# Optimization experiments

Hardware: AMD Instinct MI355X
Metric: run time of the kernel (lower is better)

Reference implementation:

```python
import jax, jax.numpy as jnp
import numpy as np

R_FACTOR = 5  # reduction factor r from Tacotron.__init__


def _gru(x, h, Wx, Wh, b):
    # standard GRU cell: z,r,candidate gates packed along last dim of Wx/Wh/b
    H = h.shape[-1]
    gx = x @ Wx
    gh = h @ Wh
    z = jax.nn.sigmoid(gx[..., :H] + gh[..., :H] + b[:H])
    r = jax.nn.sigmoid(gx[..., H:2 * H] + gh[..., H:2 * H] + b[H:2 * H])
    c = jnp.tanh(gx[..., 2 * H:] + r * gh[..., 2 * H:] + b[2 * H:])
    return (1.0 - z) * h + z * c


def setup_inputs() -> dict:
    key = jax.random.key(0)
    ks = jax.random.split(key, 16)
    T_out, B, D = 1000, 128, 80     # decoder frames, batch, mel dim
    T_in, H, P = 512, 256, 128      # encoder steps, hidden, prenet out
    n = lambda k, shp, d: jax.random.normal(k, shp, dtype=jnp.float32) * (1.0 / np.sqrt(d))
    return {
        "outputs": jax.random.normal(ks[0], (T_out, B, D), dtype=jnp.float32),
        "memory": jax.random.normal(ks[1], (T_in, B, H), dtype=jnp.float32),
        "W_pre0": n(ks[2], (D, H), D), "b_pre0": jnp.zeros((H,), jnp.float32),
        "W_pre1": n(ks[3], (H, P), H), "b_pre1": jnp.zeros((P,), jnp.float32),
        "Wx_att": n(ks[4], (P, 3 * H), P), "Wh_att": n(ks[5], (H, 3 * H), H), "b_att": jnp.zeros((3 * H,), jnp.float32),
        "Wq": n(ks[6], (H, H), H), "Wm": n(ks[7], (H, H), H), "v_att": n(ks[8], (H,), H),
        "Wx_d0": n(ks[9], (2 * H, 3 * H), 2 * H), "Wh_d0": n(ks[10], (H, 3 * H), H), "b_d0": jnp.zeros((3 * H,), jnp.float32),
        "Wx_d1": n(ks[11], (H, 3 * H), H), "Wh_d1": n(ks[12], (H, 3 * H), H), "b_d1": jnp.zeros((3 * H,), jnp.float32),
        "Wo": n(ks[13], (H, D), H), "bo": jnp.zeros((D,), jnp.float32),
    }


def _forward(outputs, memory, W_pre0, b_pre0, W_pre1, b_pre1, Wx_att, Wh_att, b_att,
             Wq, Wm, v_att, Wx_d0, Wh_d0, b_d0, Wx_d1, Wh_d1, b_d1, Wo, bo):
    r = R_FACTOR
    T_out, B, D = outputs.shape
    H = memory.shape[-1]
    R = T_out // r  # reduced_time_steps
    # teacher-forcing frame per reduced step: indic[t*r + r - 1] with r zero-frames
    # prepended == outputs[t*r - 1] for t>=1, zeros for t=0.
    frames = jnp.concatenate(
        [jnp.zeros((1, B, D), outputs.dtype), outputs[r - 1::r][: R - 1]], axis=0)  # [R,B,D]
    # precompute attention keys once (AttModule over static memory)
    keys = jnp.einsum('tbh,hk->tbk', memory, Wm)  # [T_in,B,H]
    h0 = jnp.zeros((B, H), outputs.dtype)

    def step(state, frame):
        h_att, h_d0, h_d1 = state
        # pre-net (dropout inactive: inference-mode reference)
        pre = jax.nn.relu(frame @ W_pre0 + b_pre0)
        pre = jax.nn.relu(pre @ W_pre1 + b_pre1)
        # attention RNN
        query = _gru(pre, h_att, Wx_att, Wh_att, b_att)  # [B,H]
        # additive attention
        e = jnp.einsum('tbk,k->tb', jnp.tanh(keys + query @ Wq), v_att)  # [T_in,B]
        alpha = jax.nn.softmax(e, axis=0)
        context = jnp.einsum('tb,tbh->bh', alpha, memory)  # [B,H]
        # decoder cell 0 conditioned on context, with residual from query
        out0 = _gru(jnp.concatenate([query, context], axis=-1), h_d0, Wx_d0, Wh_d0, b_d0)
        res0 = query + out0
        # residual-wrapped decoder cell 1
        out1 = _gru(res0, h_d1, Wx_d1, Wh_d1, b_d1)
        res1 = res0 + out1
        dense = res1 @ Wo + bo  # [B,D]
        return (query, out0, out1), (dense, alpha)

    _, (dense_seq, alpha_seq) = jax.lax.scan(step, (h0, h0, h0), frames)
    # each reduced-step output is written to r consecutive output frames
    final_output = jnp.repeat(dense_seq, r, axis=0)  # [T_out,B,D]
    return final_output, alpha_seq  # alpha_seq: [R,B,T_in]... axes (R,T_in,B) -> transpose


def reference(outputs, memory, W_pre0, b_pre0, W_pre1, b_pre1, Wx_att, Wh_att, b_att,
              Wq, Wm, v_att, Wx_d0, Wh_d0, b_d0, Wx_d1, Wh_d1, b_d1, Wo, bo):
    final_output, alpha_seq = _forward(outputs, memory, W_pre0, b_pre0, W_pre1, b_pre1,
                                       Wx_att, Wh_att, b_att, Wq, Wm, v_att,
                                       Wx_d0, Wh_d0, b_d0, Wx_d1, Wh_d1, b_d1, Wo, bo)
    # alpha stacked per reduced step, shape [R, T_in, B] -> [R, B, T_in] as in TF reshape
    final_alpha = jnp.transpose(alpha_seq, (0, 2, 1))
    return final_output, final_alpha
```

## Files before the change

### kernel.cpp

```cpp
#include <hip/hip_runtime.h>

namespace {
constexpr int B = 128;
constexpr int D = 80;
constexpr int H = 256;
constexpr int PP = 128;
constexpr int TIN = 512;
constexpr int RSTEPS = 200;
constexpr int RF = 5;
constexpr int HB = H * B;
}

__device__ __forceinline__ float sigm(float x) { return 1.f / (1.f + __expf(-x)); }
__device__ __forceinline__ float tanh_(float x) { return 1.f - 2.f / (__expf(2.f * x) + 1.f); }
__device__ __forceinline__ unsigned short f2bf(float f) {
  unsigned int u = __float_as_uint(f);
  u += 0x7fffu + ((u >> 16) & 1u);
  return (unsigned short)(u >> 16);
}
__device__ __forceinline__ void bf2x(unsigned int w, float& f0, float& f1) {
  f0 = __uint_as_float(w << 16);
  f1 = __uint_as_float(w & 0xffff0000u);
}
__device__ __forceinline__ void unpack8(uint4 w, float* f) {
  bf2x(w.x, f[0], f[1]); bf2x(w.y, f[2], f[3]);
  bf2x(w.z, f[4], f[5]); bf2x(w.w, f[6], f[7]);
}
__device__ __forceinline__ float dot8(uint4 w, float4 x0, float4 x1) {
  float f0, f1, a;
  bf2x(w.x, f0, f1); a  = f0 * x0.x + f1 * x0.y;
  bf2x(w.y, f0, f1); a += f0 * x0.z + f1 * x0.w;
  bf2x(w.z, f0, f1); a += f0 * x1.x + f1 * x1.y;
  bf2x(w.w, f0, f1); a += f0 * x1.z + f1 * x1.w;
  return a;
}

__global__ __launch_bounds__(256) void k_keys(const float* __restrict__ mem,
                                              const float* __restrict__ Wm,
                                              unsigned short* __restrict__ keysB) {
  const int k = threadIdx.x;
  const int m0 = blockIdx.x * 32;
  const float* xb = mem + (size_t)m0 * H;
  float acc[32];
#pragma unroll
  for (int i = 0; i < 32; ++i) acc[i] = 0.f;
  for (int h = 0; h < H; h += 4) {
    const float w0 = Wm[(h + 0) * H + k];
    const float w1 = Wm[(h + 1) * H + k];
    const float w2 = Wm[(h + 2) * H + k];
    const float w3 = Wm[(h + 3) * H + k];
#pragma unroll
    for (int mi = 0; mi < 32; ++mi) {
      const float4 x = *reinterpret_cast<const float4*>(xb + (size_t)mi * H + h);
      acc[mi] += x.x * w0 + x.y * w1 + x.z * w2 + x.w * w3;
    }
  }
#pragma unroll
  for (int mi = 0; mi < 32; ++mi) {
    const int m = m0 + mi, t = m >> 7, bb = m & 127;
    keysB[((size_t)bb * TIN + t) * H + k] = f2bf(acc[mi]);
  }
}

__global__ __launch_bounds__(256) void k_memB(const float* __restrict__ mem,
                                              unsigned short* __restrict__ memB) {
  const int m = blockIdx.x, t = m >> 7, bb = m & 127;
  memB[((size_t)bb * TIN + t) * H + threadIdx.x] = f2bf(mem[(size_t)m * H + threadIdx.x]);
}

__global__ __launch_bounds__(256) void k_packWq(const float* __restrict__ W,
                                                unsigned short* __restrict__ Wp) {
  const int idx = blockIdx.x * 256 + threadIdx.x;
  const int k = idx >> 8, c = idx & 255;
  Wp[(((size_t)(k >> 3) * 256) + c) * 8 + (k & 7)] = f2bf(W[idx]);
}

__global__ __launch_bounds__(256) void k_packG(const float* __restrict__ W,
                                               unsigned short* __restrict__ dst,
                                               int K, int rowOff) {
  const int idx = blockIdx.x * 256 + threadIdx.x;
  if (idx >= K * 768) return;
  const int k = idx / 768, c = idx - k * 768;
  const int g = c >> 8, j = c & 255;
  dst[((size_t)(rowOff + k) * 128 + (j >> 1)) * 8 + (j & 1) * 4 + g] = f2bf(W[idx]);
}

__global__ __launch_bounds__(256) void k_prenet(
    const float* __restrict__ outs, const float* __restrict__ Wp0,
    const float* __restrict__ bp0, const float* __restrict__ Wp1,
    const float* __restrict__ bp1, float* __restrict__ preT) {
  const int t = blockIdx.x >> 7, b = blockIdx.x & 127, tid = threadIdx.x;
  __shared__ float f[80];
  __shared__ float p0[256];
  __shared__ float s2[256];
  if (tid < 80)
    f[tid] = (t == 0) ? 0.f
                      : __builtin_nontemporal_load(
                            &outs[((size_t)(t * RF - 1) * B + b) * D + tid]);
  __syncthreads();
  {
    float a = bp0[tid];
#pragma unroll 8
    for (int k = 0; k < 80; ++k) a += f[k] * Wp0[k * 256 + tid];
    p0[tid] = fmaxf(a, 0.f);
  }
  __syncthreads();
  {
    const int c = tid & 127, kh = tid >> 7;
    float a = 0.f;
#pragma unroll 8
    for (int k = kh * 128; k < kh * 128 + 128; ++k) a += p0[k] * Wp1[k * 128 + c];
    s2[kh * 128 + c] = a;
  }
  __syncthreads();
  if (tid < 128)
    preT[((size_t)t * PP + tid) * B + b] = fmaxf(bp1[tid] + s2[tid] + s2[128 + tid], 0.f);
}

__device__ void gru_body(const unsigned short* __restrict__ wp, int K1, int K2,
                         int KH, const float* __restrict__ xT1,
                         const float* __restrict__ xT2,
                         const float* __restrict__ pctx0,
                         const float* __restrict__ msp,
                         const float* __restrict__ hT_old,
                         const float* __restrict__ b3, float* __restrict__ hT_new,
                         const float* __restrict__ resInT,
                         float* __restrict__ resOutT, int rel, float* smem) {
  const int tid = threadIdx.x;
  float* part = smem;
  float* red = smem + 4096;
  const int jg2 = rel >> 1, bh = rel & 1;
  const int lane = tid & 63, wv = tid >> 6;
  const int b = bh * 64 + lane;

  float c0 = 0.f, c1 = 0.f;
  if (pctx0) {
    const float m0 = msp[b], s0 = msp[B + b];
    const float m1 = msp[2 * B + b], s1 = msp[3 * B + b];
    const float M = fmaxf(m0, m1);
    const float f0 = __expf(m0 - M), f1 = __expf(m1 - M);
    const float inv = 1.f / (s0 * f0 + s1 * f1);
    c0 = f0 * inv; c1 = f1 * inv;
  }

  const uint4* wp4 = reinterpret_cast<const uint4*>(wp);
  const int K12 = K1 + K2, KT = K12 + KH;
  const int KS = KT >> 3;
  const int k0 = wv * KS, k1 = k0 + KS;

  float az0 = 0, ar0 = 0, acx0 = 0, ach0 = 0;
  float az1 = 0, ar1 = 0, acx1 = 0, ach1 = 0;
  float f0, f1;

  const int e1 = (k1 < K1) ? k1 : K1;
#pragma unroll 4
  for (int k = k0; k < e1; ++k) {
    const uint4 w = wp4[(size_t)k * 128 + jg2];
    const float x = xT1[k * B + b];
    bf2x(w.x, f0, f1); az0 += f0 * x; ar0 += f1 * x;
    bf2x(w.y, f0, f1); acx0 += f0 * x;
    bf2x(w.z, f0, f1); az1 += f0 * x; ar1 += f1 * x;
    bf2x(w.w, f0, f1); acx1 += f0 * x;
  }
  const int s2 = (k0 > K1) ? k0 : K1, e2 = (k1 < K12) ? k1 : K12;
#pragma unroll 2
  for (int k = s2; k < e2; ++k) {
    const int kk = k - K1;
    const float x = pctx0 ? (c0 * pctx0[kk * B + b] + c1 * pctx0[(256 + kk) * B + b])
                          : xT2[kk * B + b];
    const uint4 w = wp4[(size_t)k * 128 + jg2];
    bf2x(w.x, f0, f1); az0 += f0 * x; ar0 += f1 * x;
    bf2x(w.y, f0, f1); acx0 += f0 * x;
    bf2x(w.z, f0, f1); az1 += f0 * x; ar1 += f1 * x;
    bf2x(w.w, f0, f1); acx1 += f0 * x;
  }
  const int s3 = (k0 > K12) ? k0 : K12;
#pragma unroll 4
  for (int k = s3; k < k1; ++k) {
    const uint4 w = wp4[(size_t)k * 128 + jg2];
    const float x = hT_old[(k - K12) * B + b];
    bf2x(w.x, f0, f1); az0 += f0 * x; ar0 += f1 * x;
    bf2x(w.y, f0, f1); ach0 += f0 * x;
    bf2x(w.z, f0, f1); az1 += f0 * x; ar1 += f1 * x;
    bf2x(w.w, f0, f1); ach1 += f0 * x;
  }

  float* pw = part + wv * 512;
  pw[0 * 64 + lane] = az0;  pw[1 * 64 + lane] = ar0;
  pw[2 * 64 + lane] = acx0; pw[3 * 64 + lane] = ach0;
  pw[4 * 64 + lane] = az1;  pw[5 * 64 + lane] = ar1;
  pw[6 * 64 + lane] = acx1; pw[7 * 64 + lane] = ach1;
  __syncthreads();
  {
    float s = 0.f;
#pragma unroll
    for (int w = 0; w < 8; ++w) s += part[w * 512 + tid];
    red[tid] = s;
  }
  __syncthreads();
  if (tid < 128) {
    const int jl = tid >> 6, ln = tid & 63;
    const int j = jg2 * 2 + jl;
    const int bb = bh * 64 + ln;
    const float az = red[(jl * 4 + 0) * 64 + ln];
    const float ar = red[(jl * 4 + 1) * 64 + ln];
    const float acx = red[(jl * 4 + 2) * 64 + ln];
    const float ach = red[(jl * 4 + 3) * 64 + ln];
    const float z = sigm(az + b3[j]);
    const float r = sigm(ar + b3[H + j]);
    const float c = tanh_(acx + r * ach + b3[2 * H + j]);
    const float hold = hT_old[j * B + bb];
    const float hn = (1.f - z) * hold + z * c;
    hT_new[j * B + bb] = hn;
    if (resOutT) resOutT[j * B + bb] = resInT[j * B + bb] + hn;
  }
}

__device__ void dense_body(int s, int b, const float* __restrict__ res1T,
                           const float* __restrict__ Wo,
                           const float* __restrict__ bo, float* __restrict__ dout,
                           const float* __restrict__ pvalsS,
                           const float* __restrict__ msS,
                           float* __restrict__ alpha, float* smem) {
  const int tid = threadIdx.x;
  float* red = smem;
  float* part = smem + 256;
  if (tid < 256) red[tid] = res1T[tid * B + b];
  __syncthreads();
  {
    const int ks = tid >> 7, c = tid & 127;
    float a = 0.f;
    if (c < D) {
#pragma unroll 8
      for (int k = ks * 64; k < ks * 64 + 64; ++k) a += red[k] * Wo[k * D + c];
    }
    part[ks * 128 + c] = a;
  }
  __syncthreads();
  if (tid < D) {
    float dv = bo[tid];
#pragma unroll
    for (int ks = 0; ks < 4; ++ks) dv += part[ks * 128 + tid];
    const size_t base = (size_t)s * RF * (B * D) + (size_t)b * D + tid;
#pragma unroll
    for (int i = 0; i < RF; ++i)
      __builtin_nontemporal_store(dv, &dout[base + (size_t)i * (B * D)]);
  }
  const float m0 = msS[b], s0 = msS[B + b], m1 = msS[2 * B + b], s1 = msS[3 * B + b];
  const float M = fmaxf(m0, m1);
  const float f0 = __expf(m0 - M), f1 = __expf(m1 - M);
  const float inv = 1.f / (s0 * f0 + s1 * f1);
  const float cc = (tid < 256) ? f0 * inv : f1 * inv;
  __builtin_nontemporal_store(pvalsS[(size_t)b * TIN + tid] * cc,
                              &alpha[((size_t)s * B + b) * TIN + tid]);
}

__device__ void attn_half_body(int b, int half, const float* __restrict__ qT,
                               const unsigned short* __restrict__ wqB,
                               const float* __restrict__ v_att,
                               const unsigned short* __restrict__ keysB,
                               const unsigned short* __restrict__ memB,
                               float* __restrict__ pvalsS, float* __restrict__ pctxS,
                               float* __restrict__ msS, float* smem) {
  const int tid = threadIdx.x;
  const int lane = tid & 63, wv = tid >> 6;
  const int t0 = half * 256;
  float* hA = smem;
  float* qk_p = smem + 256;
  float* v_p = smem + 544;
  float* scr = smem + 832;
  float* ep = smem + 4928;
  float* r16 = smem + 5184;
  float* bc = smem + 5200;

  if (tid < 256) {
    hA[tid] = qT[tid * B + b];
    v_p[(tid >> 4) * 18 + (tid & 15)] = v_att[tid];
  }
  __syncthreads();
  const float4* hA4 = reinterpret_cast<const float4*>(hA);
  const uint4* wQ = reinterpret_cast<const uint4*>(wqB);

  {
    const int c = tid & 255, ks = tid >> 8;
    float a = 0.f;
#pragma unroll
    for (int q = 0; q < 16; ++q) {
      const int kg = ks * 16 + q;
      a += dot8(wQ[(size_t)kg * 256 + c], hA4[kg * 2], hA4[kg * 2 + 1]);
    }
    scr[ks * 256 + c] = a;
  }
  __syncthreads();
  if (tid < 256)
    qk_p[(tid >> 4) * 18 + (tid & 15)] = scr[tid] + scr[256 + tid];
  __syncthreads();

  {
    const int l16 = tid & 15, g = tid >> 4;
    float qg[16], vg[16];
#pragma unroll
    for (int i = 0; i < 16; ++i) {
      qg[i] = qk_p[l16 * 18 + i];
      vg[i] = v_p[l16 * 18 + i];
    }
    const uint4* kB = reinterpret_cast<const uint4*>(keysB + (size_t)b * TIN * H);
#pragma unroll
    for (int p = 0; p < 4; ++p) {
      const int r1 = g + p * 64, r2 = r1 + 32;
      const uint4 a0 = kB[(size_t)(t0 + r1) * 32 + l16 * 2];
      const uint4 a1 = kB[(size_t)(t0 + r1) * 32 + l16 * 2 + 1];
      const uint4 b0 = kB[(size_t)(t0 + r2) * 32 + l16 * 2];
      const uint4 b1 = kB[(size_t)(t0 + r2) * 32 + l16 * 2 + 1];
      float ka[16], kb2[16];
      unpack8(a0, ka); unpack8(a1, ka + 8);
      unpack8(b0, kb2); unpack8(b1, kb2 + 8);
      float s1 = 0.f, s2 = 0.f;
#pragma unroll
      for (int i = 0; i < 16; ++i) {
        s1 += vg[i] * tanh_(ka[i] + qg[i]);
        s2 += vg[i] * tanh_(kb2[i] + qg[i]);
      }
#pragma unroll
      for (int m = 1; m < 16; m <<= 1) { s1 += __shfl_xor(s1, m, 16); s2 += __shfl_xor(s2, m, 16); }
      if (l16 == 0) { ep[r1] = s1; ep[r2] = s2; }
    }
  }
  __syncthreads();

  float ev = -1e30f, pv = 0.f;
  if (tid < 256) {
    ev = ep[tid];
    float mx = ev;
#pragma unroll
    for (int m = 1; m < 64; m <<= 1) mx = fmaxf(mx, __shfl_xor(mx, m));
    if (lane == 0) r16[wv] = mx;
  }
  __syncthreads();
  if (tid == 0)
    bc[0] = fmaxf(fmaxf(r16[0], r16[1]), fmaxf(r16[2], r16[3]));
  __syncthreads();
  const float M = bc[0];
  if (tid < 256) {
    pv = __expf(ev - M);
    ep[tid] = pv;
    pvalsS[(size_t)b * TIN + t0 + tid] = pv;
    float s = pv;
#pragma unroll
    for (int m = 1; m < 64; m <<= 1) s += __shfl_xor(s, m);
    if (lane == 0) r16[wv] = s;
  }
  __syncthreads();
  if (tid == 0) {
    msS[half * 2 * B + b] = M;
    msS[(half * 2 + 1) * B + b] = r16[0] + r16[1] + r16[2] + r16[3];
  }

  {
    const int kq8 = tid & 31, ts = tid >> 5;
    float a[8] = {0.f, 0.f, 0.f, 0.f, 0.f, 0.f, 0.f, 0.f};
    const uint4* mB = reinterpret_cast<const uint4*>(memB + (size_t)b * TIN * H);
#pragma unroll 4
    for (int i = 0; i < 16; ++i) {
      const int tt = ts * 16 + i;
      const float p = ep[tt];
      float mv[8];
      unpack8(mB[(size_t)(t0 + tt) * 32 + kq8], mv);
#pragma unroll
      for (int j = 0; j < 8; ++j) a[j] += p * mv[j];
    }
    float4* s4 = reinterpret_cast<float4*>(scr + ts * 256 + kq8 * 8);
    s4[0] = make_float4(a[0], a[1], a[2], a[3]);
    s4[1] = make_float4(a[4], a[5], a[6], a[7]);
  }
  __syncthreads();
  if (tid < 256) {
    float s = 0.f;
#pragma unroll
    for (int ts2 = 0; ts2 < 16; ++ts2) s += scr[ts2 * 256 + tid];
    pctxS[(size_t)(half * 256 + tid) * B + b] = s;
  }
}

__global__ __launch_bounds__(512, 8) void k_pipe(
    int i, const unsigned short* __restrict__ wgA,
    const unsigned short* __restrict__ wg0, const unsigned short* __restrict__ wg1,
    const unsigned short* __restrict__ wqB, const float* __restrict__ v_att,
    const float* __restrict__ b_att, const float* __restrict__ b_d0,
    const float* __restrict__ b_d1, const unsigned short* __restrict__ keysB,
    const unsigned short* __restrict__ memB, const float* __restrict__ preT,
    float* __restrict__ qr, float* __restrict__ hd0r, float* __restrict__ hd1r,
    float* __restrict__ res0r, float* __restrict__ res1r,
    float* __restrict__ pvals, float* __restrict__ pctx, float* __restrict__ ms,
    const float* __restrict__ Wo, const float* __restrict__ bo,
    float* __restrict__ dout, float* __restrict__ alpha) {
  __shared__ alignas(16) float smem[5248];
  const int blk = blockIdx.x;
  if (blk < 256) {
    const int t = i - 1;
    if (t >= 0 && t < RSTEPS) {
      const int sl = t & 3;
      attn_half_body(blk >> 1, blk & 1, qr + (size_t)sl * HB, wqB, v_att, keysB,
                     memB, pvals + (size_t)sl * B * TIN,
                     pctx + (size_t)sl * 2 * HB, ms + (size_t)sl * 4 * B, smem);
    }
  } else if (blk < 512) {
    const int t = i;
    if (t < RSTEPS)
      gru_body(wgA, PP, 0, H, preT + (size_t)t * PP * B, nullptr, nullptr,
               nullptr, qr + (size_t)((t + 3) & 3) * HB, b_att,
               qr + (size_t)(t & 3) * HB, nullptr, nullptr, blk - 256, smem);
  } else if (blk < 768) {
    const int t = i - 2;
    if (t >= 0 && t < RSTEPS) {
      const int sl = t & 3;
      gru_body(wg0, H, H, H, qr + (size_t)sl * HB, nullptr,
               pctx + (size_t)sl * 2 * HB, ms + (size_t)sl * 4 * B,
               hd0r + (size_t)((t + 3) & 3) * HB, b_d0,
               hd0r + (size_t)sl * HB, qr + (size_t)sl * HB,
               res0r + (size_t)sl * HB, blk - 512, smem);
    }
  } else if (blk < 1024) {
    const int t = i - 3;
    if (t >= 0 && t < RSTEPS) {
      const int sl = t & 3;
      gru_body(wg1, H, 0, H, res0r + (size_t)sl * HB, nullptr, nullptr, nullptr,
               hd1r + (size_t)((t + 3) & 3) * HB, b_d1, hd1r + (size_t)sl * HB,
               res0r + (size_t)sl * HB, res1r + (size_t)sl * HB, blk - 768, smem);
    }
  } else {
    const int t = i - 4;
    if (t >= 0 && t < RSTEPS) {
      const int sl = t & 3;
      dense_body(t, blk - 1024, res1r + (size_t)sl * HB, Wo, bo, dout,
                 pvals + (size_t)sl * B * TIN, ms + (size_t)sl * 4 * B, alpha,
                 smem);
    }
  }
}

extern "C" void kernel_launch(void* const* d_in, const int* in_sizes, int n_in,
                              void* d_out, int out_size, void* d_ws,
                              size_t ws_size, hipStream_t stream) {
  const float* outs   = (const float*)d_in[0];
  const float* memory = (const float*)d_in[1];
  const float* Wp0    = (const float*)d_in[2];
  const float* bp0    = (const float*)d_in[3];
  const float* Wp1    = (const float*)d_in[4];
  const float* bp1    = (const float*)d_in[5];
  const float* Wx_att = (const float*)d_in[6];
  const float* Wh_att = (const float*)d_in[7];
  const float* b_att  = (const float*)d_in[8];
  const float* Wq     = (const float*)d_in[9];
  const float* Wm     = (const float*)d_in[10];
  const float* v_att  = (const float*)d_in[11];
  const float* Wx_d0  = (const float*)d_in[12];
  const float* Wh_d0  = (const float*)d_in[13];
  const float* b_d0   = (const float*)d_in[14];
  const float* Wx_d1  = (const float*)d_in[15];
  const float* Wh_d1  = (const float*)d_in[16];
  const float* b_d1   = (const float*)d_in[17];
  const float* Wo     = (const float*)d_in[18];
  const float* bo     = (const float*)d_in[19];
  float* dout = (float*)d_out;
  float* wsf  = (float*)d_ws;

  size_t off = 0;
  unsigned short* keysB = (unsigned short*)(wsf + off); off += (size_t)TIN * B * H / 2;
  unsigned short* memB  = (unsigned short*)(wsf + off); off += (size_t)TIN * B * H / 2;
  unsigned short* wqB   = (unsigned short*)(wsf + off); off += (size_t)256 * 256 / 2;
  unsigned short* wgA   = (unsigned short*)(wsf + off); off += (size_t)384 * 1024 / 2;
  unsigned short* wg0   = (unsigned short*)(wsf + off); off += (size_t)768 * 1024 / 2;
  unsigned short* wg1   = (unsigned short*)(wsf + off); off += (size_t)512 * 1024 / 2;
  float* preT  = wsf + off; off += (size_t)RSTEPS * PP * B;
  float* qr    = wsf + off; off += (size_t)4 * HB;
  float* hd0r  = wsf + off; off += (size_t)4 * HB;
  float* hd1r  = wsf + off; off += (size_t)4 * HB;
  float* res0r = wsf + off; off += (size_t)4 * HB;
  float* res1r = wsf + off; off += (size_t)4 * HB;
  float* pvals = wsf + off; off += (size_t)4 * B * TIN;
  float* pctx  = wsf + off; off += (size_t)4 * 2 * HB;
  float* ms    = wsf + off; off += (size_t)4 * 4 * B;

  hipMemsetAsync(qr + 3 * HB, 0, (size_t)HB * sizeof(float), stream);
  hipMemsetAsync(hd0r + 3 * HB, 0, (size_t)HB * sizeof(float), stream);
  hipMemsetAsync(hd1r + 3 * HB, 0, (size_t)HB * sizeof(float), stream);

  k_keys<<<(TIN * B) / 32, 256, 0, stream>>>(memory, Wm, keysB);
  k_memB<<<TIN * B, 256, 0, stream>>>(memory, memB);
  k_prenet<<<RSTEPS * B, 256, 0, stream>>>(outs, Wp0, bp0, Wp1, bp1, preT);
  k_packWq<<<256, 256, 0, stream>>>(Wq, wqB);
  k_packG<<<(128 * 768 + 255) / 256, 256, 0, stream>>>(Wx_att, wgA, 128, 0);
  k_packG<<<(256 * 768 + 255) / 256, 256, 0, stream>>>(Wh_att, wgA, 256, 128);
  k_packG<<<(512 * 768 + 255) / 256, 256, 0, stream>>>(Wx_d0, wg0, 512, 0);
  k_packG<<<(256 * 768 + 255) / 256, 256, 0, stream>>>(Wh_d0, wg0, 256, 512);
  k_packG<<<(256 * 768 + 255) / 256, 256, 0, stream>>>(Wx_d1, wg1, 256, 0);
  k_packG<<<(256 * 768 + 255) / 256, 256, 0, stream>>>(Wh_d1, wg1, 256, 256);

  float* alpha = dout + (size_t)1000 * B * D;

  for (int i = 0; i < RSTEPS + 4; ++i) {
    k_pipe<<<1152, 512, 0, stream>>>(i, wgA, wg0, wg1, wqB, v_att, b_att,
                                     b_d0, b_d1, keysB, memB, preT, qr, hd0r,
                                     hd1r, res0r, res1r, pvals, pctx, ms, Wo,
                                     bo, dout, alpha);
  }
}
```

Before: 7.792 ms.

## Fuse memB conversion into keys kernel and halve decoder-1 GRU block count

The keys projection kernel now also writes the bf16 copy of memory, and its blocks are reindexed per batch row so both outputs are stored contiguously. This removes the separate memB kernel and a second read of memory. The GRU body is templated on the number of column pairs per block: decoder cell 1 uses two pairs, so it needs 128 blocks instead of 256, and the block-role order in the pipeline kernel changes. The pipeline grid shrinks from 1152 to 1024 blocks, but static shared memory grows and the decoder-1 blocks carry twice the accumulators, which may lengthen that stage of the step.

```diff
diff --git a/kernel.cpp b/kernel.cpp
--- a/kernel.cpp
+++ b/kernel.cpp
@@ -37,10 +37,11 @@
 
 __global__ __launch_bounds__(256) void k_keys(const float* __restrict__ mem,
                                               const float* __restrict__ Wm,
-                                              unsigned short* __restrict__ keysB) {
+                                              unsigned short* __restrict__ keysB,
+                                              unsigned short* __restrict__ memB) {
   const int k = threadIdx.x;
-  const int m0 = blockIdx.x * 32;
-  const float* xb = mem + (size_t)m0 * H;
+  const int bb = blockIdx.x >> 4, t0 = (blockIdx.x & 15) * 32;
+  const float* base = mem + (size_t)t0 * (B * H) + (size_t)bb * H;
   float acc[32];
 #pragma unroll
   for (int i = 0; i < 32; ++i) acc[i] = 0.f;
@@ -50,22 +51,17 @@
     const float w2 = Wm[(h + 2) * H + k];
     const float w3 = Wm[(h + 3) * H + k];
 #pragma unroll
-    for (int mi = 0; mi < 32; ++mi) {
-      const float4 x = *reinterpret_cast<const float4*>(xb + (size_t)mi * H + h);
-      acc[mi] += x.x * w0 + x.y * w1 + x.z * w2 + x.w * w3;
-    }
-  }
-#pragma unroll
-  for (int mi = 0; mi < 32; ++mi) {
-    const int m = m0 + mi, t = m >> 7, bb = m & 127;
-    keysB[((size_t)bb * TIN + t) * H + k] = f2bf(acc[mi]);
-  }
-}
-
-__global__ __launch_bounds__(256) void k_memB(const float* __restrict__ mem,
-                                              unsigned short* __restrict__ memB) {
-  const int m = blockIdx.x, t = m >> 7, bb = m & 127;
-  memB[((size_t)bb * TIN + t) * H + threadIdx.x] = f2bf(mem[(size_t)m * H + threadIdx.x]);
+    for (int ti = 0; ti < 32; ++ti) {
+      const float4 x = *reinterpret_cast<const float4*>(base + (size_t)ti * (B * H) + h);
+      acc[ti] += x.x * w0 + x.y * w1 + x.z * w2 + x.w * w3;
+    }
+  }
+#pragma unroll
+  for (int ti = 0; ti < 32; ++ti) {
+    const size_t o = ((size_t)bb * TIN + t0 + ti) * H + k;
+    keysB[o] = f2bf(acc[ti]);
+    memB[o] = f2bf(base[(size_t)ti * (B * H) + k]);
+  }
 }
 
 __global__ __launch_bounds__(256) void k_packWq(const float* __restrict__ W,
@@ -117,6 +113,7 @@
     preT[((size_t)t * PP + tid) * B + b] = fmaxf(bp1[tid] + s2[tid] + s2[128 + tid], 0.f);
 }
 
+template <int NJP>
 __device__ void gru_body(const unsigned short* __restrict__ wp, int K1, int K2,
                          int KH, const float* __restrict__ xT1,
                          const float* __restrict__ xT2,
@@ -128,8 +125,8 @@
                          float* __restrict__ resOutT, int rel, float* smem) {
   const int tid = threadIdx.x;
   float* part = smem;
-  float* red = smem + 4096;
-  const int jg2 = rel >> 1, bh = rel & 1;
+  float* red = smem + 8 * NJP * 512;
+  const int grp = rel >> 1, bh = rel & 1;
   const int lane = tid & 63, wv = tid >> 6;
   const int b = bh * 64 + lane;
 
@@ -138,9 +135,9 @@
     const float m0 = msp[b], s0 = msp[B + b];
     const float m1 = msp[2 * B + b], s1 = msp[3 * B + b];
     const float M = fmaxf(m0, m1);
-    const float f0 = __expf(m0 - M), f1 = __expf(m1 - M);
-    const float inv = 1.f / (s0 * f0 + s1 * f1);
-    c0 = f0 * inv; c1 = f1 * inv;
+    const float e0 = __expf(m0 - M), e1 = __expf(m1 - M);
+    const float inv = 1.f / (s0 * e0 + s1 * e1);
+    c0 = e0 * inv; c1 = e1 * inv;
   }
 
   const uint4* wp4 = reinterpret_cast<const uint4*>(wp);
@@ -148,59 +145,65 @@
   const int KS = KT >> 3;
   const int k0 = wv * KS, k1 = k0 + KS;
 
-  float az0 = 0, ar0 = 0, acx0 = 0, ach0 = 0;
-  float az1 = 0, ar1 = 0, acx1 = 0, ach1 = 0;
+  float acc[NJP * 8];
+#pragma unroll
+  for (int i = 0; i < NJP * 8; ++i) acc[i] = 0.f;
   float f0, f1;
 
-  const int e1 = (k1 < K1) ? k1 : K1;
-#pragma unroll 4
-  for (int k = k0; k < e1; ++k) {
-    const uint4 w = wp4[(size_t)k * 128 + jg2];
+#define UPD(wq, xv, base, CS)                                                  \
+  bf2x(wq.x, f0, f1); acc[base + 0] += f0 * xv; acc[base + 1] += f1 * xv;      \
+  bf2x(wq.y, f0, f1); acc[base + CS] += f0 * xv;                               \
+  bf2x(wq.z, f0, f1); acc[base + 4] += f0 * xv; acc[base + 5] += f1 * xv;      \
+  bf2x(wq.w, f0, f1); acc[base + 4 + CS] += f0 * xv;
+
+  const int e1i = (k1 < K1) ? k1 : K1;
+#pragma unroll 2
+  for (int k = k0; k < e1i; ++k) {
     const float x = xT1[k * B + b];
-    bf2x(w.x, f0, f1); az0 += f0 * x; ar0 += f1 * x;
-    bf2x(w.y, f0, f1); acx0 += f0 * x;
-    bf2x(w.z, f0, f1); az1 += f0 * x; ar1 += f1 * x;
-    bf2x(w.w, f0, f1); acx1 += f0 * x;
-  }
-  const int s2 = (k0 > K1) ? k0 : K1, e2 = (k1 < K12) ? k1 : K12;
+#pragma unroll
+    for (int p = 0; p < NJP; ++p) {
+      const uint4 w = wp4[(size_t)k * 128 + grp * NJP + p];
+      UPD(w, x, p * 8, 2)
+    }
+  }
+  const int s2i = (k0 > K1) ? k0 : K1, e2i = (k1 < K12) ? k1 : K12;
 #pragma unroll 2
-  for (int k = s2; k < e2; ++k) {
+  for (int k = s2i; k < e2i; ++k) {
     const int kk = k - K1;
     const float x = pctx0 ? (c0 * pctx0[kk * B + b] + c1 * pctx0[(256 + kk) * B + b])
                           : xT2[kk * B + b];
-    const uint4 w = wp4[(size_t)k * 128 + jg2];
-    bf2x(w.x, f0, f1); az0 += f0 * x; ar0 += f1 * x;
-    bf2x(w.y, f0, f1); acx0 += f0 * x;
-    bf2x(w.z, f0, f1); az1 += f0 * x; ar1 += f1 * x;
-    bf2x(w.w, f0, f1); acx1 += f0 * x;
-  }
-  const int s3 = (k0 > K12) ? k0 : K12;
-#pragma unroll 4
-  for (int k = s3; k < k1; ++k) {
-    const uint4 w = wp4[(size_t)k * 128 + jg2];
+#pragma unroll
+    for (int p = 0; p < NJP; ++p) {
+      const uint4 w = wp4[(size_t)k * 128 + grp * NJP + p];
+      UPD(w, x, p * 8, 2)
+    }
+  }
+  const int s3i = (k0 > K12) ? k0 : K12;
+#pragma unroll 2
+  for (int k = s3i; k < k1; ++k) {
     const float x = hT_old[(k - K12) * B + b];
-    bf2x(w.x, f0, f1); az0 += f0 * x; ar0 += f1 * x;
-    bf2x(w.y, f0, f1); ach0 += f0 * x;
-    bf2x(w.z, f0, f1); az1 += f0 * x; ar1 += f1 * x;
-    bf2x(w.w, f0, f1); ach1 += f0 * x;
-  }
-
-  float* pw = part + wv * 512;
-  pw[0 * 64 + lane] = az0;  pw[1 * 64 + lane] = ar0;
-  pw[2 * 64 + lane] = acx0; pw[3 * 64 + lane] = ach0;
-  pw[4 * 64 + lane] = az1;  pw[5 * 64 + lane] = ar1;
-  pw[6 * 64 + lane] = acx1; pw[7 * 64 + lane] = ach1;
-  __syncthreads();
-  {
+#pragma unroll
+    for (int p = 0; p < NJP; ++p) {
+      const uint4 w = wp4[(size_t)k * 128 + grp * NJP + p];
+      UPD(w, x, p * 8, 3)
+    }
+  }
+#undef UPD
+
+  float* pw = part + wv * (NJP * 512);
+#pragma unroll
+  for (int i = 0; i < NJP * 8; ++i) pw[i * 64 + lane] = acc[i];
+  __syncthreads();
+  for (int idx = tid; idx < NJP * 512; idx += 512) {
     float s = 0.f;
 #pragma unroll
-    for (int w = 0; w < 8; ++w) s += part[w * 512 + tid];
-    red[tid] = s;
-  }
-  __syncthreads();
-  if (tid < 128) {
+    for (int w = 0; w < 8; ++w) s += part[w * (NJP * 512) + idx];
+    red[idx] = s;
+  }
+  __syncthreads();
+  if (tid < NJP * 128) {
     const int jl = tid >> 6, ln = tid & 63;
-    const int j = jg2 * 2 + jl;
+    const int j = grp * (NJP * 2) + jl;
     const int bb = bh * 64 + ln;
     const float az = red[(jl * 4 + 0) * 64 + ln];
     const float ar = red[(jl * 4 + 1) * 64 + ln];
@@ -394,7 +397,7 @@
     float* __restrict__ pvals, float* __restrict__ pctx, float* __restrict__ ms,
     const float* __restrict__ Wo, const float* __restrict__ bo,
     float* __restrict__ dout, float* __restrict__ alpha) {
-  __shared__ alignas(16) float smem[5248];
+  __shared__ alignas(16) float smem[9216];
   const int blk = blockIdx.x;
   if (blk < 256) {
     const int t = i - 1;
@@ -405,34 +408,35 @@
                      pctx + (size_t)sl * 2 * HB, ms + (size_t)sl * 4 * B, smem);
     }
   } else if (blk < 512) {
-    const int t = i;
-    if (t < RSTEPS)
-      gru_body(wgA, PP, 0, H, preT + (size_t)t * PP * B, nullptr, nullptr,
-               nullptr, qr + (size_t)((t + 3) & 3) * HB, b_att,
-               qr + (size_t)(t & 3) * HB, nullptr, nullptr, blk - 256, smem);
-  } else if (blk < 768) {
     const int t = i - 2;
     if (t >= 0 && t < RSTEPS) {
       const int sl = t & 3;
-      gru_body(wg0, H, H, H, qr + (size_t)sl * HB, nullptr,
-               pctx + (size_t)sl * 2 * HB, ms + (size_t)sl * 4 * B,
-               hd0r + (size_t)((t + 3) & 3) * HB, b_d0,
-               hd0r + (size_t)sl * HB, qr + (size_t)sl * HB,
-               res0r + (size_t)sl * HB, blk - 512, smem);
-    }
-  } else if (blk < 1024) {
+      gru_body<1>(wg0, H, H, H, qr + (size_t)sl * HB, nullptr,
+                  pctx + (size_t)sl * 2 * HB, ms + (size_t)sl * 4 * B,
+                  hd0r + (size_t)((t + 3) & 3) * HB, b_d0,
+                  hd0r + (size_t)sl * HB, qr + (size_t)sl * HB,
+                  res0r + (size_t)sl * HB, blk - 256, smem);
+    }
+  } else if (blk < 768) {
+    const int t = i;
+    if (t < RSTEPS)
+      gru_body<1>(wgA, PP, 0, H, preT + (size_t)t * PP * B, nullptr, nullptr,
+                  nullptr, qr + (size_t)((t + 3) & 3) * HB, b_att,
+                  qr + (size_t)(t & 3) * HB, nullptr, nullptr, blk - 512, smem);
+  } else if (blk < 896) {
     const int t = i - 3;
     if (t >= 0 && t < RSTEPS) {
       const int sl = t & 3;
-      gru_body(wg1, H, 0, H, res0r + (size_t)sl * HB, nullptr, nullptr, nullptr,
-               hd1r + (size_t)((t + 3) & 3) * HB, b_d1, hd1r + (size_t)sl * HB,
-               res0r + (size_t)sl * HB, res1r + (size_t)sl * HB, blk - 768, smem);
+      gru_body<2>(wg1, H, 0, H, res0r + (size_t)sl * HB, nullptr, nullptr,
+                  nullptr, hd1r + (size_t)((t + 3) & 3) * HB, b_d1,
+                  hd1r + (size_t)sl * HB, res0r + (size_t)sl * HB,
+                  res1r + (size_t)sl * HB, blk - 768, smem);
     }
   } else {
     const int t = i - 4;
     if (t >= 0 && t < RSTEPS) {
       const int sl = t & 3;
-      dense_body(t, blk - 1024, res1r + (size_t)sl * HB, Wo, bo, dout,
+      dense_body(t, blk - 896, res1r + (size_t)sl * HB, Wo, bo, dout,
                  pvals + (size_t)sl * B * TIN, ms + (size_t)sl * 4 * B, alpha,
                  smem);
     }
@@ -486,8 +490,7 @@
   hipMemsetAsync(hd0r + 3 * HB, 0, (size_t)HB * sizeof(float), stream);
   hipMemsetAsync(hd1r + 3 * HB, 0, (size_t)HB * sizeof(float), stream);
 
-  k_keys<<<(TIN * B) / 32, 256, 0, stream>>>(memory, Wm, keysB);
-  k_memB<<<TIN * B, 256, 0, stream>>>(memory, memB);
+  k_keys<<<B * 16, 256, 0, stream>>>(memory, Wm, keysB, memB);
   k_prenet<<<RSTEPS * B, 256, 0, stream>>>(outs, Wp0, bp0, Wp1, bp1, preT);
   k_packWq<<<256, 256, 0, stream>>>(Wq, wqB);
   k_packG<<<(128 * 768 + 255) / 256, 256, 0, stream>>>(Wx_att, wgA, 128, 0);
@@ -500,7 +503,7 @@
   float* alpha = dout + (size_t)1000 * B * D;
 
   for (int i = 0; i < RSTEPS + 4; ++i) {
-    k_pipe<<<1152, 512, 0, stream>>>(i, wgA, wg0, wg1, wqB, v_att, b_att,
+    k_pipe<<<1024, 512, 0, stream>>>(i, wgA, wg0, wg1, wqB, v_att, b_att,
                                      b_d0, b_d1, keysB, memB, preT, qr, hd0r,
                                      hd1r, res0r, res1r, pvals, pctx, ms, Wo,
                                      bo, dout, alpha);
```

Result: faster. 7.502 ms (-3.7%).
